# Optimization experiments

Measured on AMD Instinct MI355X. Metric: run time of the kernel, lower is better.

## Reference

```python
import jax, jax.numpy as jnp
import numpy as np

LN_EPS = 1e-5

def _layer_norm(x):
    m = jnp.mean(x, axis=-1, keepdims=True)
    v = jnp.mean(jnp.square(x - m), axis=-1, keepdims=True)
    return (x - m) / jnp.sqrt(v + LN_EPS)

def setup_inputs() -> dict:
    key = jax.random.key(0)
    ks = jax.random.split(key, 6)
    B, S, d_in, d_out = 8, 2048, 1024, 4096
    x = jax.random.normal(ks[0], (B, S, d_in), dtype=jnp.float32)
    # torch.randn % 1 -> values in [0, 1)
    weight_in = jax.random.uniform(ks[1], (d_out, d_in), dtype=jnp.float32)
    bias_in = jax.random.uniform(ks[2], (d_out,), dtype=jnp.float32)
    weight_out = jax.random.uniform(ks[3], (d_in, d_out), dtype=jnp.float32)
    bias_out = jax.random.uniform(ks[4], (d_in,), dtype=jnp.float32)
    lengths = jax.random.randint(ks[5], (B,), 1, S + 1, dtype=jnp.int64 if jax.config.read('jax_enable_x64') else jnp.int32)
    return {"x": x, "weight_in": weight_in, "bias_in": bias_in,
            "weight_out": weight_out, "bias_out": bias_out, "lengths": lengths}

def reference(x, weight_in, bias_in, weight_out, bias_out, lengths):
    # lengths is unused mathematically in the dense baseline (ragged kernels
    # only skip padded rows; valid-region math identical).
    for _ in range(10):
        x = jnp.einsum('bsd,od->bso', x, weight_in) + bias_in  # [B,S,d_out]
        x = _layer_norm(x)
        x = jnp.einsum('bso,do->bsd', x, weight_out) + bias_out  # [B,S,d_in]
        x = _layer_norm(x)
    return x
```

## Files before the change

kernel.cpp:

```cpp
#include <hip/hip_runtime.h>


typedef __attribute__((ext_vector_type(4))) float    f32x4;
typedef __attribute__((ext_vector_type(8))) _Float16 f16x8;
typedef __attribute__((ext_vector_type(4))) _Float16 f16x4;

#define LN_EPS 1e-5f

__device__ __forceinline__ ushort f2h_bits(float f) {
    union { _Float16 h; ushort u; } c; c.h = (_Float16)f; return c.u;
}

typedef const __attribute__((address_space(1))) void* gas_ptr;
typedef __attribute__((address_space(3))) void* las_ptr;

__device__ __forceinline__ void gload_lds16(const void* g, void* l) {
    __builtin_amdgcn_global_load_lds((gas_ptr)g, (las_ptr)l, 16, 0, 0);
}

__device__ __forceinline__ f16x8 ldf(const _Float16* base, int byteoff) {
    return *reinterpret_cast<const f16x8*>(
        reinterpret_cast<const char*>(base) + byteoff);
}

__global__ __launch_bounds__(256) void conv_f32_f16(
        const float* __restrict__ in, _Float16* __restrict__ outp, int n4) {
    int i = blockIdx.x * 256 + threadIdx.x;
    if (i >= n4) return;
    float4 f = reinterpret_cast<const float4*>(in)[i];
    f16x4 r;
    r[0] = (_Float16)f.x; r[1] = (_Float16)f.y;
    r[2] = (_Float16)f.z; r[3] = (_Float16)f.w;
    *reinterpret_cast<f16x4*>(&outp[(size_t)i * 4]) = r;
}

template<int W>
__global__ __launch_bounds__(256)
void rowsum_rows(const _Float16* __restrict__ w, float* __restrict__ outp) {
    const int wid  = threadIdx.x >> 6;
    const int lane = threadIdx.x & 63;
    const size_t row = (size_t)blockIdx.x * 4 + wid;
    const _Float16* p = w + row * W;
    float s = 0.f;
    #pragma unroll
    for (int i = 0; i < W / 512; ++i) {
        f16x8 v = *reinterpret_cast<const f16x8*>(p + i * 512 + lane * 8);
        #pragma unroll
        for (int j = 0; j < 8; ++j) s += (float)v[j];
    }
    #pragma unroll
    for (int off = 32; off > 0; off >>= 1) s += __shfl_xor(s, off);
    if (lane == 0) outp[row] = s;
}

__global__ __launch_bounds__(256) void init_ident_stats(float2* __restrict__ st) {
    int i = blockIdx.x * 256 + threadIdx.x;
    st[i] = make_float2(0.f, 1.f);
}

template<int NP, int W>
__global__ __launch_bounds__(256)
void reduce_stats(const float2* __restrict__ part, float2* __restrict__ st) {
    const int wid  = threadIdx.x >> 6;
    const int lane = threadIdx.x & 63;
    const size_t row = (size_t)blockIdx.x * 4 + wid;
    float s = 0.f, q = 0.f;
    if (lane < NP) {
        float2 p = part[row * NP + lane];
        s = p.x; q = p.y;
    }
    #pragma unroll
    for (int off = 32; off > 0; off >>= 1) {
        s += __shfl_xor(s, off);
        q += __shfl_xor(q, off);
    }
    if (lane == 0) {
        const float mean = s * (1.0f / W);
        const float var  = fmaxf(q * (1.0f / W) - mean * mean, 0.f);
        st[row] = make_float2(mean, rsqrtf(var + LN_EPS));
    }
}

template<int M, int N, int K>
__global__ __launch_bounds__(512)
void gemm256_ln(const _Float16* __restrict__ A, const _Float16* __restrict__ B,
                const float* __restrict__ bias, const float* __restrict__ wsum,
                const float2* __restrict__ stats, _Float16* __restrict__ C,
                float2* __restrict__ partials) {
    constexpr int NT  = K / 64;
    constexpr int NIT = NT / 2;
    constexpr int NBX = N / 256;
    constexpr int NWG = (M / 256) * NBX;
    constexpr int NPART = NBX * 4;

    __shared__ __attribute__((aligned(16))) _Float16 lds[2][2][2][8192];

    const int tid  = threadIdx.x;
    const int wid  = tid >> 6;
    const int lane = tid & 63;
    const int wr   = wid >> 2;
    const int wc   = wid & 3;

    int bn0, bm0;
    if constexpr (NBX == 16) {
        const int x = blockIdx.x & 7, j = blockIdx.x >> 3;
        bn0 = (x * 2 + (j & 1)) * 256;
        bm0 = (j >> 1) * 256;
    } else {
        int bid = (blockIdx.x & 7) * (NWG >> 3) + (blockIdx.x >> 3);
        bn0 = (bid % NBX) * 256;
        bm0 = (bid / NBX) * 256;
    }

    const int trow = tid >> 3;
    const int cg   = (tid & 7) ^ (trow & 7);
    const _Float16* Asrc = A + (size_t)(bm0 + trow) * K + cg * 8;
    const _Float16* Bsrc = B + (size_t)(bn0 + trow) * K + cg * 8;

    const int fr  = lane & 15;
    const int fq  = lane >> 4;
    const int s8  = lane & 7;
    const int cb0 = ((fq       ^ s8) << 4);
    const int cb1 = (((4 + fq) ^ s8) << 4);
    const int brb = (wc & 1) * 64;

    const _Float16* Ah[2] = { &lds[0][0][wr][0],      &lds[1][0][wr][0] };
    const _Float16* Bh[2] = { &lds[0][1][wc >> 1][0], &lds[1][1][wc >> 1][0] };

    f32x4 acc[8][4] = {};
    f16x8 aLo[4][2], aHi[4][2], bLo[2][2], bHi[2][2];

#define STAGE_A(buf, h, kts) do { \
    gload_lds16(Asrc + (size_t)((h)*128     ) * K + (kts), (void*)&lds[buf][0][h][       wid*512]); \
    gload_lds16(Asrc + (size_t)((h)*128 + 64) * K + (kts), (void*)&lds[buf][0][h][4096 + wid*512]); } while(0)
#define STAGE_B(buf, h, kts) do { \
    gload_lds16(Bsrc + (size_t)((h)*128     ) * K + (kts), (void*)&lds[buf][1][h][       wid*512]); \
    gload_lds16(Bsrc + (size_t)((h)*128 + 64) * K + (kts), (void*)&lds[buf][1][h][4096 + wid*512]); } while(0)

#define READ_ALO(b) do { _Pragma("unroll") for (int i = 0; i < 4; ++i) { \
    aLo[i][0] = ldf(Ah[b], (i*16+fr)*128 + cb0); \
    aLo[i][1] = ldf(Ah[b], (i*16+fr)*128 + cb1); } } while(0)
#define READ_AHI(b) do { _Pragma("unroll") for (int i = 0; i < 4; ++i) { \
    aHi[i][0] = ldf(Ah[b], ((i+4)*16+fr)*128 + cb0); \
    aHi[i][1] = ldf(Ah[b], ((i+4)*16+fr)*128 + cb1); } } while(0)
#define READ_BLO(b) do { _Pragma("unroll") for (int j = 0; j < 2; ++j) { \
    bLo[j][0] = ldf(Bh[b], (brb + j*16 + fr)*128 + cb0); \
    bLo[j][1] = ldf(Bh[b], (brb + j*16 + fr)*128 + cb1); } } while(0)
#define READ_BHI(b) do { _Pragma("unroll") for (int j = 0; j < 2; ++j) { \
    bHi[j][0] = ldf(Bh[b], (brb + (j+2)*16 + fr)*128 + cb0); \
    bHi[j][1] = ldf(Bh[b], (brb + (j+2)*16 + fr)*128 + cb1); } } while(0)

#define MFMA_BLK(AF, ioff, BF, joff) do { \
    _Pragma("unroll") for (int i = 0; i < 4; ++i) \
    _Pragma("unroll") for (int j = 0; j < 2; ++j) { \
        acc[i+ioff][j+joff] = __builtin_amdgcn_mfma_f32_16x16x32_f16(AF[i][0], BF[j][0], acc[i+ioff][j+joff], 0, 0, 0); \
        acc[i+ioff][j+joff] = __builtin_amdgcn_mfma_f32_16x16x32_f16(AF[i][1], BF[j][1], acc[i+ioff][j+joff], 0, 0, 0); } } while(0)

#define BARRIER() __builtin_amdgcn_s_barrier()
#define VMCNT4()  asm volatile("s_waitcnt vmcnt(4)" ::: "memory")

    STAGE_B(0, 0, 0);  STAGE_B(0, 1, 0);
    STAGE_A(0, 0, 0);  STAGE_A(0, 1, 0);
    STAGE_B(1, 0, 64); STAGE_B(1, 1, 64);
    VMCNT4();
    BARRIER();

    for (int it = 0; it < NIT; ++it) {
        const int k1 = it * 128 + 64;
        const int k2 = (it * 128 + 128) & (K - 1);
        const int k3 = (it * 128 + 192) & (K - 1);

        READ_ALO(0); READ_BLO(0);
        STAGE_A(1, 0, k1);
        BARRIER();
        __builtin_amdgcn_s_setprio(1); MFMA_BLK(aLo, 0, bLo, 0); __builtin_amdgcn_s_setprio(0);
        BARRIER();
        READ_BHI(0);
        STAGE_A(1, 1, k1);
        BARRIER();
        __builtin_amdgcn_s_setprio(1); MFMA_BLK(aLo, 0, bHi, 2); __builtin_amdgcn_s_setprio(0);
        BARRIER();
        READ_AHI(0);
        STAGE_B(0, 0, k2);
        BARRIER();
        __builtin_amdgcn_s_setprio(1); MFMA_BLK(aHi, 4, bLo, 0); __builtin_amdgcn_s_setprio(0);
        BARRIER();
        STAGE_B(0, 1, k2);
        BARRIER();
        __builtin_amdgcn_s_setprio(1); MFMA_BLK(aHi, 4, bHi, 2); __builtin_amdgcn_s_setprio(0);
        VMCNT4();
        BARRIER();
        READ_ALO(1); READ_BLO(1);
        STAGE_A(0, 0, k2);
        BARRIER();
        __builtin_amdgcn_s_setprio(1); MFMA_BLK(aLo, 0, bLo, 0); __builtin_amdgcn_s_setprio(0);
        BARRIER();
        READ_BHI(1);
        STAGE_A(0, 1, k2);
        BARRIER();
        __builtin_amdgcn_s_setprio(1); MFMA_BLK(aLo, 0, bHi, 2); __builtin_amdgcn_s_setprio(0);
        BARRIER();
        READ_AHI(1);
        STAGE_B(1, 0, k3);
        BARRIER();
        __builtin_amdgcn_s_setprio(1); MFMA_BLK(aHi, 4, bLo, 0); __builtin_amdgcn_s_setprio(0);
        BARRIER();
        STAGE_B(1, 1, k3);
        BARRIER();
        __builtin_amdgcn_s_setprio(1); MFMA_BLK(aHi, 4, bHi, 2); __builtin_amdgcn_s_setprio(0);
        VMCNT4();
        BARRIER();
    }

    asm volatile("s_waitcnt vmcnt(0)" ::: "memory");
    __syncthreads();

    float bcol[4], wcol[4];
    #pragma unroll
    for (int j = 0; j < 4; ++j) {
        const int c = bn0 + wc * 64 + j * 16 + fr;
        bcol[j] = bias[c];
        wcol[j] = wsum[c];
    }

    ushort* eps = (ushort*)&lds[0][0][0][0];
    #pragma unroll
    for (int i = 0; i < 8; ++i) {
        #pragma unroll
        for (int q = 0; q < 4; ++q) {
            const int rloc = wr * 128 + i * 16 + fq * 4 + q;
            const float2 st = stats[bm0 + rloc];
            const float rs = st.y, coef = st.y * st.x;
            const int key = (((rloc >> 2) & 3) << 4);
            float s = 0.f, sq = 0.f;
            #pragma unroll
            for (int j = 0; j < 4; ++j) {
                const float v = rs * acc[i][j][q] - coef * wcol[j] + bcol[j];
                s += v; sq += v * v;
                const int c = wc * 64 + j * 16 + fr;
                eps[rloc * 256 + (c ^ key)] = f2h_bits(v);
            }
            #pragma unroll
            for (int off = 1; off < 16; off <<= 1) {
                s  += __shfl_xor(s,  off);
                sq += __shfl_xor(sq, off);
            }
            if (fr == 0)
                partials[(size_t)(bm0 + rloc) * NPART + (bn0 >> 8) * 4 + wc] =
                    make_float2(s, sq);
        }
    }
    __syncthreads();

    {
        const int g  = tid >> 4;
        const int q4 = (tid >> 2) & 3;
        const int a  = tid & 3;
        const int rb = (g >> 2) * 16 + q4 * 4 + (g & 3);
        const int keyx = q4 << 4;
        #pragma unroll
        for (int h = 0; h < 2; ++h) {
            const int r = rb + h * 128;
            const ushort* rp = eps + r * 256;
            _Float16* cp = C + (size_t)(bm0 + r) * N + bn0;
            #pragma unroll
            for (int k = 0; k < 8; ++k) {
                const int col = (4 * k + a) * 8;
                *reinterpret_cast<uint4*>((ushort*)cp + col) =
                    *reinterpret_cast<const uint4*>(rp + (col ^ keyx));
            }
        }
    }
#undef STAGE_A
#undef STAGE_B
#undef READ_ALO
#undef READ_AHI
#undef READ_BLO
#undef READ_BHI
#undef MFMA_BLK
#undef BARRIER
#undef VMCNT4
}

__global__ __launch_bounds__(256)
void ln_final(const _Float16* __restrict__ a, const float2* __restrict__ st,
              float* __restrict__ outp) {
    const int wid  = threadIdx.x >> 6;
    const int lane = threadIdx.x & 63;
    const size_t row = (size_t)blockIdx.x * 4 + wid;
    const float2 s = st[row];
    const float mean = s.x, rstd = s.y;
    const _Float16* p = a + row * 1024;
    #pragma unroll
    for (int i = 0; i < 2; ++i) {
        f16x8 v = *reinterpret_cast<const f16x8*>(p + i * 512 + lane * 8);
        float* op = outp + row * 1024 + i * 512 + lane * 8;
        float4 o0, o1;
        o0.x = ((float)v[0] - mean) * rstd;
        o0.y = ((float)v[1] - mean) * rstd;
        o0.z = ((float)v[2] - mean) * rstd;
        o0.w = ((float)v[3] - mean) * rstd;
        o1.x = ((float)v[4] - mean) * rstd;
        o1.y = ((float)v[5] - mean) * rstd;
        o1.z = ((float)v[6] - mean) * rstd;
        o1.w = ((float)v[7] - mean) * rstd;
        reinterpret_cast<float4*>(op)[0] = o0;
        reinterpret_cast<float4*>(op)[1] = o1;
    }
}

extern "C" void kernel_launch(void* const* d_in, const int* in_sizes, int n_in,
                              void* d_out, int out_size, void* d_ws, size_t ws_size,
                              hipStream_t stream) {
    const float* x     = (const float*)d_in[0];
    const float* w_in  = (const float*)d_in[1];
    const float* b_in  = (const float*)d_in[2];
    const float* w_out = (const float*)d_in[3];
    const float* b_out = (const float*)d_in[4];

    constexpr int Mrows = 16384;
    constexpr int Din   = 1024;
    constexpr int Dout  = 4096;

    char* ws = (char*)d_ws;
    _Float16* wib = (_Float16*)ws; ws += (size_t)Dout * Din * 2;
    _Float16* wob = (_Float16*)ws; ws += (size_t)Din * Dout * 2;
    _Float16* a2b = (_Float16*)ws; ws += (size_t)Mrows * Din * 2;
    _Float16* a1b = (_Float16*)ws; ws += (size_t)Mrows * Dout * 2;
    float* winsum  = (float*)ws;   ws += Dout * 4;
    float* woutsum = (float*)ws;   ws += Din * 4;
    float2* st1 = (float2*)ws;     ws += (size_t)Mrows * 8;
    float2* st2 = (float2*)ws;     ws += (size_t)Mrows * 8;
    float2* p1  = (float2*)ws;     ws += (size_t)Mrows * 64 * 8;
    float2* p2  = (float2*)ws;

    const dim3 blk(256);

    conv_f32_f16<<<(Dout * Din / 4) / 256, blk, 0, stream>>>(w_in,  wib, Dout * Din / 4);
    conv_f32_f16<<<(Din * Dout / 4) / 256, blk, 0, stream>>>(w_out, wob, Din * Dout / 4);
    conv_f32_f16<<<(Mrows * Din / 4) / 256, blk, 0, stream>>>(x, a2b, Mrows * Din / 4);
    rowsum_rows<Din> <<<Dout / 4, blk, 0, stream>>>(wib, winsum);
    rowsum_rows<Dout><<<Din / 4,  blk, 0, stream>>>(wob, woutsum);
    init_ident_stats<<<Mrows / 128, blk, 0, stream>>>(st2);

    for (int it = 0; it < 10; ++it) {
        gemm256_ln<Mrows, Dout, Din>
            <<<(Mrows / 256) * (Dout / 256), dim3(512), 0, stream>>>(
                a2b, wib, b_in, winsum, st2, a1b, p1);
        reduce_stats<64, Dout><<<Mrows / 4, blk, 0, stream>>>(p1, st1);
        gemm256_ln<Mrows, Din, Dout>
            <<<(Mrows / 256) * (Din / 256), dim3(512), 0, stream>>>(
                a1b, wob, b_out, woutsum, st1, a2b, p2);
        reduce_stats<16, Din><<<Mrows / 4, blk, 0, stream>>>(p2, st2);
    }
    ln_final<<<Mrows / 4, blk, 0, stream>>>(a2b, st2, (float*)d_out);
}
```

Before: 3.058 ms.

## Make first GEMM persistent over four M-panels and restructure the LN epilogue

```diff
diff --git a/kernel.cpp b/kernel.cpp
--- a/kernel.cpp
+++ b/kernel.cpp
@@ -81,17 +81,17 @@
     }
 }
 
-template<int M, int N, int K>
+template<int M, int N, int K, int PANELS>
 __global__ __launch_bounds__(512)
 void gemm256_ln(const _Float16* __restrict__ A, const _Float16* __restrict__ B,
                 const float* __restrict__ bias, const float* __restrict__ wsum,
                 const float2* __restrict__ stats, _Float16* __restrict__ C,
                 float2* __restrict__ partials) {
-    constexpr int NT  = K / 64;
-    constexpr int NIT = NT / 2;
-    constexpr int NBX = N / 256;
-    constexpr int NWG = (M / 256) * NBX;
-    constexpr int NPART = NBX * 4;
+    constexpr int NT     = K / 64;
+    constexpr int NIT    = NT / 2;
+    constexpr int NBX    = N / 256;
+    constexpr int NTILES = PANELS * NT;
+    constexpr int NWG    = (M / (256 * PANELS)) * NBX;
 
     __shared__ __attribute__((aligned(16))) _Float16 lds[2][2][2][8192];
 
@@ -101,20 +101,19 @@
     const int wr   = wid >> 2;
     const int wc   = wid & 3;
 
-    int bn0, bm0;
+    int bn0, bm0b;
     if constexpr (NBX == 16) {
         const int x = blockIdx.x & 7, j = blockIdx.x >> 3;
-        bn0 = (x * 2 + (j & 1)) * 256;
-        bm0 = (j >> 1) * 256;
+        bn0  = (x * 2 + (j & 1)) * 256;
+        bm0b = (j >> 1) * (256 * PANELS);
     } else {
         int bid = (blockIdx.x & 7) * (NWG >> 3) + (blockIdx.x >> 3);
-        bn0 = (bid % NBX) * 256;
-        bm0 = (bid / NBX) * 256;
+        bn0  = (bid % NBX) * 256;
+        bm0b = (bid / NBX) * (256 * PANELS);
     }
 
     const int trow = tid >> 3;
     const int cg   = (tid & 7) ^ (trow & 7);
-    const _Float16* Asrc = A + (size_t)(bm0 + trow) * K + cg * 8;
     const _Float16* Bsrc = B + (size_t)(bn0 + trow) * K + cg * 8;
 
     const int fr  = lane & 15;
@@ -127,15 +126,16 @@
     const _Float16* Ah[2] = { &lds[0][0][wr][0],      &lds[1][0][wr][0] };
     const _Float16* Bh[2] = { &lds[0][1][wc >> 1][0], &lds[1][1][wc >> 1][0] };
 
-    f32x4 acc[8][4] = {};
-    f16x8 aLo[4][2], aHi[4][2], bLo[2][2], bHi[2][2];
-
-#define STAGE_A(buf, h, kts) do { \
-    gload_lds16(Asrc + (size_t)((h)*128     ) * K + (kts), (void*)&lds[buf][0][h][       wid*512]); \
-    gload_lds16(Asrc + (size_t)((h)*128 + 64) * K + (kts), (void*)&lds[buf][0][h][4096 + wid*512]); } while(0)
-#define STAGE_B(buf, h, kts) do { \
-    gload_lds16(Bsrc + (size_t)((h)*128     ) * K + (kts), (void*)&lds[buf][1][h][       wid*512]); \
-    gload_lds16(Bsrc + (size_t)((h)*128 + 64) * K + (kts), (void*)&lds[buf][1][h][4096 + wid*512]); } while(0)
+#define STAGE_A(buf, h, t) do { \
+    const int _tt = (t) & (NTILES - 1); \
+    const _Float16* _as = A + (size_t)(bm0b + (_tt / NT) * 256 + (h) * 128 + trow) * K \
+                            + (_tt % NT) * 64 + cg * 8; \
+    gload_lds16(_as,                  (void*)&lds[buf][0][h][       wid*512]); \
+    gload_lds16(_as + (size_t)64 * K, (void*)&lds[buf][0][h][4096 + wid*512]); } while(0)
+#define STAGE_B(buf, h, t) do { \
+    const int _kk = ((t) & (NT - 1)) * 64; \
+    gload_lds16(Bsrc + (size_t)((h)*128     ) * K + _kk, (void*)&lds[buf][1][h][       wid*512]); \
+    gload_lds16(Bsrc + (size_t)((h)*128 + 64) * K + _kk, (void*)&lds[buf][1][h][4096 + wid*512]); } while(0)
 
 #define READ_ALO(b) do { _Pragma("unroll") for (int i = 0; i < 4; ++i) { \
     aLo[i][0] = ldf(Ah[b], (i*16+fr)*128 + cb0); \
@@ -159,116 +159,118 @@
 #define BARRIER() __builtin_amdgcn_s_barrier()
 #define VMCNT4()  asm volatile("s_waitcnt vmcnt(4)" ::: "memory")
 
-    STAGE_B(0, 0, 0);  STAGE_B(0, 1, 0);
-    STAGE_A(0, 0, 0);  STAGE_A(0, 1, 0);
-    STAGE_B(1, 0, 64); STAGE_B(1, 1, 64);
+    STAGE_B(0, 0, 0); STAGE_B(0, 1, 0);
+    STAGE_A(0, 0, 0); STAGE_A(0, 1, 0);
+    STAGE_B(1, 0, 1); STAGE_B(1, 1, 1);
     VMCNT4();
     BARRIER();
 
-    for (int it = 0; it < NIT; ++it) {
-        const int k1 = it * 128 + 64;
-        const int k2 = (it * 128 + 128) & (K - 1);
-        const int k3 = (it * 128 + 192) & (K - 1);
-
-        READ_ALO(0); READ_BLO(0);
-        STAGE_A(1, 0, k1);
-        BARRIER();
-        __builtin_amdgcn_s_setprio(1); MFMA_BLK(aLo, 0, bLo, 0); __builtin_amdgcn_s_setprio(0);
-        BARRIER();
-        READ_BHI(0);
-        STAGE_A(1, 1, k1);
-        BARRIER();
-        __builtin_amdgcn_s_setprio(1); MFMA_BLK(aLo, 0, bHi, 2); __builtin_amdgcn_s_setprio(0);
-        BARRIER();
-        READ_AHI(0);
-        STAGE_B(0, 0, k2);
-        BARRIER();
-        __builtin_amdgcn_s_setprio(1); MFMA_BLK(aHi, 4, bLo, 0); __builtin_amdgcn_s_setprio(0);
-        BARRIER();
-        STAGE_B(0, 1, k2);
-        BARRIER();
-        __builtin_amdgcn_s_setprio(1); MFMA_BLK(aHi, 4, bHi, 2); __builtin_amdgcn_s_setprio(0);
-        VMCNT4();
-        BARRIER();
-        READ_ALO(1); READ_BLO(1);
-        STAGE_A(0, 0, k2);
-        BARRIER();
-        __builtin_amdgcn_s_setprio(1); MFMA_BLK(aLo, 0, bLo, 0); __builtin_amdgcn_s_setprio(0);
-        BARRIER();
-        READ_BHI(1);
-        STAGE_A(0, 1, k2);
-        BARRIER();
-        __builtin_amdgcn_s_setprio(1); MFMA_BLK(aLo, 0, bHi, 2); __builtin_amdgcn_s_setprio(0);
-        BARRIER();
-        READ_AHI(1);
-        STAGE_B(1, 0, k3);
-        BARRIER();
-        __builtin_amdgcn_s_setprio(1); MFMA_BLK(aHi, 4, bLo, 0); __builtin_amdgcn_s_setprio(0);
-        BARRIER();
-        STAGE_B(1, 1, k3);
-        BARRIER();
-        __builtin_amdgcn_s_setprio(1); MFMA_BLK(aHi, 4, bHi, 2); __builtin_amdgcn_s_setprio(0);
-        VMCNT4();
-        BARRIER();
-    }
-
-    asm volatile("s_waitcnt vmcnt(0)" ::: "memory");
-    __syncthreads();
-
     float bcol[4], wcol[4];
     #pragma unroll
     for (int j = 0; j < 4; ++j) {
         const int c = bn0 + wc * 64 + j * 16 + fr;
-        bcol[j] = bias[c];
-        wcol[j] = wsum[c];
-    }
-
-    ushort* eps = (ushort*)&lds[0][0][0][0];
-    #pragma unroll
-    for (int i = 0; i < 8; ++i) {
+        bcol[j] = bias[c]; wcol[j] = wsum[c];
+    }
+
+    for (int p = 0; p < PANELS; ++p) {
+        f32x4 acc[8][4] = {};
+        f16x8 aLo[4][2], aHi[4][2], bLo[2][2], bHi[2][2];
+
+        for (int it = 0; it < NIT; ++it) {
+            const int T = p * NT + 2 * it;
+            READ_ALO(0); READ_BLO(0);
+            STAGE_A(1, 0, T + 1);
+            BARRIER();
+            __builtin_amdgcn_s_setprio(1); MFMA_BLK(aLo, 0, bLo, 0); __builtin_amdgcn_s_setprio(0);
+            BARRIER();
+            READ_BHI(0);
+            STAGE_A(1, 1, T + 1);
+            BARRIER();
+            __builtin_amdgcn_s_setprio(1); MFMA_BLK(aLo, 0, bHi, 2); __builtin_amdgcn_s_setprio(0);
+            BARRIER();
+            READ_AHI(0);
+            STAGE_B(0, 0, T + 2);
+            BARRIER();
+            __builtin_amdgcn_s_setprio(1); MFMA_BLK(aHi, 4, bLo, 0); __builtin_amdgcn_s_setprio(0);
+            BARRIER();
+            STAGE_B(0, 1, T + 2);
+            BARRIER();
+            __builtin_amdgcn_s_setprio(1); MFMA_BLK(aHi, 4, bHi, 2); __builtin_amdgcn_s_setprio(0);
+            VMCNT4();
+            BARRIER();
+            READ_ALO(1); READ_BLO(1);
+            STAGE_A(0, 0, T + 2);
+            BARRIER();
+            __builtin_amdgcn_s_setprio(1); MFMA_BLK(aLo, 0, bLo, 0); __builtin_amdgcn_s_setprio(0);
+            BARRIER();
+            READ_BHI(1);
+            STAGE_A(0, 1, T + 2);
+            BARRIER();
+            __builtin_amdgcn_s_setprio(1); MFMA_BLK(aLo, 0, bHi, 2); __builtin_amdgcn_s_setprio(0);
+            BARRIER();
+            READ_AHI(1);
+            STAGE_B(1, 0, T + 3);
+            BARRIER();
+            __builtin_amdgcn_s_setprio(1); MFMA_BLK(aHi, 4, bLo, 0); __builtin_amdgcn_s_setprio(0);
+            BARRIER();
+            STAGE_B(1, 1, T + 3);
+            BARRIER();
+            __builtin_amdgcn_s_setprio(1); MFMA_BLK(aHi, 4, bHi, 2); __builtin_amdgcn_s_setprio(0);
+            VMCNT4();
+            BARRIER();
+        }
+
+        const int bm0 = bm0b + p * 256;
+        ushort* eps = (ushort*)&lds[1][0][0][0];
         #pragma unroll
-        for (int q = 0; q < 4; ++q) {
-            const int rloc = wr * 128 + i * 16 + fq * 4 + q;
-            const float2 st = stats[bm0 + rloc];
-            const float rs = st.y, coef = st.y * st.x;
-            const int key = (((rloc >> 2) & 3) << 4);
-            float s = 0.f, sq = 0.f;
-            #pragma unroll
-            for (int j = 0; j < 4; ++j) {
-                const float v = rs * acc[i][j][q] - coef * wcol[j] + bcol[j];
-                s += v; sq += v * v;
-                const int c = wc * 64 + j * 16 + fr;
-                eps[rloc * 256 + (c ^ key)] = f2h_bits(v);
+        for (int pass = 0; pass < 4; ++pass) {
+            if (wr == (pass >> 1)) {
+                #pragma unroll
+                for (int i2 = 0; i2 < 4; ++i2) {
+                    const int i = (pass & 1) * 4 + i2;
+                    #pragma unroll
+                    for (int q = 0; q < 4; ++q) {
+                        const int rloc = wr * 128 + i * 16 + fq * 4 + q;
+                        const int rl   = rloc - pass * 64;
+                        const float2 st = stats[bm0 + rloc];
+                        const float rs = st.y, coef = st.y * st.x;
+                        const int key = ((rl >> 2) & 3) << 4;
+                        #pragma unroll
+                        for (int j = 0; j < 4; ++j) {
+                            const float v = rs * acc[i][j][q] - coef * wcol[j] + bcol[j];
+                            const int c = wc * 64 + j * 16 + fr;
+                            eps[rl * 256 + (c ^ key)] = f2h_bits(v);
+                        }
+                    }
+                }
             }
-            #pragma unroll
-            for (int off = 1; off < 16; off <<= 1) {
-                s  += __shfl_xor(s,  off);
-                sq += __shfl_xor(sq, off);
+            BARRIER();
+            {
+                const int rl  = tid >> 3;
+                const int a8  = tid & 7;
+                const int r   = bm0 + pass * 64 + rl;
+                const int key = ((rl >> 2) & 3) << 4;
+                float s = 0.f, sq = 0.f;
+                ushort* crow = (ushort*)(C + (size_t)r * N + bn0);
+                #pragma unroll
+                for (int k = 0; k < 4; ++k) {
+                    const int ch = 8 * k + a8;
+                    uint4 d = *reinterpret_cast<const uint4*>(&eps[rl * 256 + ch * 8]);
+                    f16x8 v = *reinterpret_cast<const f16x8*>(&d);
+                    #pragma unroll
+                    for (int e = 0; e < 8; ++e) {
+                        const float f = (float)v[e];
+                        s += f; sq += f * f;
+                    }
+                    *reinterpret_cast<uint4*>(&crow[(ch * 8) ^ key]) = d;
+                }
+                s  += __shfl_xor(s, 1);  sq += __shfl_xor(sq, 1);
+                s  += __shfl_xor(s, 2);  sq += __shfl_xor(sq, 2);
+                s  += __shfl_xor(s, 4);  sq += __shfl_xor(sq, 4);
+                if (a8 == 0)
+                    partials[(size_t)r * NBX + (bn0 >> 8)] = make_float2(s, sq);
             }
-            if (fr == 0)
-                partials[(size_t)(bm0 + rloc) * NPART + (bn0 >> 8) * 4 + wc] =
-                    make_float2(s, sq);
-        }
-    }
-    __syncthreads();
-
-    {
-        const int g  = tid >> 4;
-        const int q4 = (tid >> 2) & 3;
-        const int a  = tid & 3;
-        const int rb = (g >> 2) * 16 + q4 * 4 + (g & 3);
-        const int keyx = q4 << 4;
-        #pragma unroll
-        for (int h = 0; h < 2; ++h) {
-            const int r = rb + h * 128;
-            const ushort* rp = eps + r * 256;
-            _Float16* cp = C + (size_t)(bm0 + r) * N + bn0;
-            #pragma unroll
-            for (int k = 0; k < 8; ++k) {
-                const int col = (4 * k + a) * 8;
-                *reinterpret_cast<uint4*>((ushort*)cp + col) =
-                    *reinterpret_cast<const uint4*>(rp + (col ^ keyx));
-            }
+            BARRIER();
         }
     }
 #undef STAGE_A
@@ -331,7 +333,7 @@
     float* woutsum = (float*)ws;   ws += Din * 4;
     float2* st1 = (float2*)ws;     ws += (size_t)Mrows * 8;
     float2* st2 = (float2*)ws;     ws += (size_t)Mrows * 8;
-    float2* p1  = (float2*)ws;     ws += (size_t)Mrows * 64 * 8;
+    float2* p1  = (float2*)ws;     ws += (size_t)Mrows * 16 * 8;
     float2* p2  = (float2*)ws;
 
     const dim3 blk(256);
@@ -344,14 +346,12 @@
     init_ident_stats<<<Mrows / 128, blk, 0, stream>>>(st2);
 
     for (int it = 0; it < 10; ++it) {
-        gemm256_ln<Mrows, Dout, Din>
-            <<<(Mrows / 256) * (Dout / 256), dim3(512), 0, stream>>>(
-                a2b, wib, b_in, winsum, st2, a1b, p1);
-        reduce_stats<64, Dout><<<Mrows / 4, blk, 0, stream>>>(p1, st1);
-        gemm256_ln<Mrows, Din, Dout>
-            <<<(Mrows / 256) * (Din / 256), dim3(512), 0, stream>>>(
-                a1b, wob, b_out, woutsum, st1, a2b, p2);
-        reduce_stats<16, Din><<<Mrows / 4, blk, 0, stream>>>(p2, st2);
+        gemm256_ln<Mrows, Dout, Din, 4>
+            <<<256, dim3(512), 0, stream>>>(a2b, wib, b_in, winsum, st2, a1b, p1);
+        reduce_stats<16, Dout><<<Mrows / 4, blk, 0, stream>>>(p1, st1);
+        gemm256_ln<Mrows, Din, Dout, 1>
+            <<<256, dim3(512), 0, stream>>>(a1b, wob, b_out, woutsum, st1, a2b, p2);
+        reduce_stats<4, Din><<<Mrows / 4, blk, 0, stream>>>(p2, st2);
     }
     ln_final<<<Mrows / 4, blk, 0, stream>>>(a2b, st2, (float*)d_out);
 }
```

Result: slower. 4.139 ms (+35.3%).
